# Performance work log

Measured on AMD Instinct MI355X. Metric: run time of the kernel, lower is better.

Reference implementation:

```python
import jax, jax.numpy as jnp
import numpy as np

SEQ_LEN, BATCH, VOCAB, EMB, HID, NUM_LAYERS = 128, 64, 10000, 512, 512, 2


def setup_inputs() -> dict:
    key = jax.random.key(0)
    ks = jax.random.split(key, 16)
    b = float(np.sqrt(1.0 / HID))  # Linear init bound per init_weights_uniform
    u = lambda k, shape, bound: jax.random.uniform(k, shape, jnp.float32, -bound, bound)
    L = NUM_LAYERS - 1
    return {
        "inputs": jax.random.randint(ks[0], (SEQ_LEN, BATCH), 0, VOCAB, dtype=jnp.int32),
        "hidden": jnp.zeros((NUM_LAYERS, BATCH, HID), jnp.float32),
        "emb": u(ks[1], (VOCAB, EMB), 0.1),
        "W_ih0": u(ks[2], (HID, EMB), b),
        "b_ih0": u(ks[3], (HID,), b),
        "W_hh0": u(ks[4], (HID, HID), b),
        "b_hh0": u(ks[5], (HID,), b),
        "W_in": u(ks[6], (L, HID, HID), b),
        "b_in": u(ks[7], (L, HID), b),
        "W_hh": u(ks[8], (L, HID, HID), b),
        "b_hh": u(ks[9], (L, HID), b),
        "Wy": u(ks[10], (VOCAB, HID), 0.1),
        "by": jnp.zeros((VOCAB,), jnp.float32),
    }


def reference(inputs, hidden, emb, W_ih0, b_ih0, W_hh0, b_hh0,
              W_in, b_in, W_hh, b_hh, Wy, by):
    n_extra = W_in.shape[0]  # num_layers - 1 (static)

    def step(h, x_t):
        # h: [L, B, H]; x_t: [B] int tokens
        e = emb[x_t]  # [B, E]
        h0 = jnp.tanh(e @ W_ih0.T + b_ih0 + h[0] @ W_hh0.T + b_hh0)
        hs = [h0]
        for l in range(n_extra):  # small static layer loop
            hl = jnp.tanh(hs[-1] @ W_in[l].T + b_in[l]
                          + h[l + 1] @ W_hh[l].T + b_hh[l])
            hs.append(hl)
        h_new = jnp.stack(hs)  # [L, B, H]
        logits_t = hs[-1] @ Wy.T + by  # [B, V]
        return h_new, logits_t

    hidden_final, logits = jax.lax.scan(step, hidden, inputs)
    return logits, hidden_final  # [S, B, V], [L, B, H]
```

## Files before the change

### kernel.cpp

```cpp
#include <hip/hip_runtime.h>
#include <hip/hip_bf16.h>

#define SEQ 128
#define BAT 64
#define VOC 10000
#define EMBD 512
#define HID 512
#define BH (BAT*HID)
#define PRE0_OFF 0
#define H0_OFF   ((size_t)SEQ*BH)
#define H1_OFF   (H0_OFF + (size_t)(SEQ+1)*BH)
#define FLAGS_OFF (H1_OFF + (size_t)(SEQ+1)*BH)
#define CONV_OFF (FLAGS_OFF + 256)
#define LOGITS_N ((size_t)SEQ*BAT*VOC)
#define CONV_USHORTS 5382144ull
#define WS_NEED_FLOATS (CONV_OFF + CONV_USHORTS/2)

typedef __attribute__((ext_vector_type(8))) __bf16 bf16x8;
typedef __attribute__((ext_vector_type(4))) float f32x4;

__global__ __launch_bounds__(256) void init_state_k(const float* __restrict__ hidden,
                                                    float* __restrict__ h0_0,
                                                    float* __restrict__ h1_0,
                                                    unsigned* __restrict__ flags) {
    int i = blockIdx.x * 256 + threadIdx.x;
    if (i < 256) flags[i] = 0u;
    if (i < BH) { h0_0[i] = hidden[i]; h1_0[i] = hidden[BH + i]; }
}

__global__ __launch_bounds__(256) void gemm_nt_k(
    const float* __restrict__ A, const int* __restrict__ tok,
    const float* __restrict__ Bm,
    const float* __restrict__ bias0, const float* __restrict__ bias1,
    float* __restrict__ C, int N, int K, int ldc)
{
    __shared__ float As[32][132];
    __shared__ float Bs[32][132];
    __shared__ int toks[128];

    const int tid = threadIdx.x;
    const int r0 = blockIdx.x * 128;
    const int c0 = blockIdx.y * 128;

    if (tok != nullptr && tid < 128) toks[tid] = tok[r0 + tid];
    __syncthreads();

    const int tn = tid & 15;
    const int tm = tid >> 4;
    const int m0 = tm * 8, n0 = tn * 8;

    float acc[8][8];
#pragma unroll
    for (int i = 0; i < 8; ++i)
#pragma unroll
        for (int j = 0; j < 8; ++j) acc[i][j] = 0.f;

    for (int k0 = 0; k0 < K; k0 += 32) {
#pragma unroll
        for (int p = 0; p < 4; ++p) {
            int idx = p * 256 + tid;
            int row = idx >> 3;
            int kq  = (idx & 7) << 2;
            size_t arow = tok ? (size_t)toks[row] : (size_t)(r0 + row);
            float4 a = *(const float4*)(A + arow * (size_t)K + k0 + kq);
            As[kq+0][row] = a.x; As[kq+1][row] = a.y;
            As[kq+2][row] = a.z; As[kq+3][row] = a.w;
            int gc = c0 + row;
            float4 b = make_float4(0.f, 0.f, 0.f, 0.f);
            if (gc < N) b = *(const float4*)(Bm + (size_t)gc * K + k0 + kq);
            Bs[kq+0][row] = b.x; Bs[kq+1][row] = b.y;
            Bs[kq+2][row] = b.z; Bs[kq+3][row] = b.w;
        }
        __syncthreads();
#pragma unroll 8
        for (int k = 0; k < 32; ++k) {
            float4 a0 = *(const float4*)&As[k][m0];
            float4 a1 = *(const float4*)&As[k][m0 + 4];
            float4 b0 = *(const float4*)&Bs[k][n0];
            float4 b1 = *(const float4*)&Bs[k][n0 + 4];
            float am[8] = {a0.x,a0.y,a0.z,a0.w,a1.x,a1.y,a1.z,a1.w};
            float bn[8] = {b0.x,b0.y,b0.z,b0.w,b1.x,b1.y,b1.z,b1.w};
#pragma unroll
            for (int i = 0; i < 8; ++i)
#pragma unroll
                for (int j = 0; j < 8; ++j) acc[i][j] += am[i] * bn[j];
        }
        __syncthreads();
    }

    const bool full = (c0 + 128 <= N);
#pragma unroll
    for (int i = 0; i < 8; ++i) {
        size_t r = (size_t)(r0 + m0 + i);
        float* crow = C + r * (size_t)ldc;
#pragma unroll
        for (int j = 0; j < 8; ++j) {
            int c = c0 + n0 + j;
            if (full || c < N) {
                float v = acc[i][j];
                if (bias0) v += bias0[c];
                if (bias1) v += bias1[c];
                crow[c] = v;
            }
        }
    }
}

#define BFLY(S, N)                                                     \
    {                                                                  \
        _Pragma("unroll")                                              \
        for (int i = 0; i < N; ++i) {                                  \
            float lo_ = a[i], hi_ = a[i + N];                          \
            float send_ = (lane & S) ? lo_ : hi_;                      \
            float recv_ = __shfl_xor(send_, S);                       \
            a[i] = ((lane & S) ? hi_ : lo_) + recv_;                   \
        }                                                              \
    }

__global__ __launch_bounds__(512) void recurrence_k(
    const float* __restrict__ pre0, const float* __restrict__ W_hh0,
    const float* __restrict__ W_in, const float* __restrict__ b_in,
    const float* __restrict__ W_hh, const float* __restrict__ b_hh,
    float* __restrict__ h0_all, float* __restrict__ h1_all,
    unsigned* __restrict__ flags)
{
    __shared__ float xs[16384];

    const int tid  = threadIdx.x;
    const int lane = tid & 63;
    const int wv   = tid >> 6;
    const int p = ((lane&1)<<5)|((lane&2)<<3)|((lane&4)<<1)
                | ((lane&8)>>1)|((lane&16)>>3)|((lane&32)>>5);
    const int b_own = p >> 3, j_own = p & 7;

    unsigned* fl1 = flags;
    unsigned* fl2 = flags + 64;

    float4 wr[8][2];
    float a[64];

    if (blockIdx.x < 64) {
        const int g = blockIdx.x >> 4, jb = blockIdx.x & 15;
        const int bt = wv & 1, jt = wv >> 1;
        const size_t win = (size_t)(g << 4) * HID;
#pragma unroll
        for (int jj = 0; jj < 8; ++jj) {
            const float* wp = W_hh0 + (size_t)(jb*32 + jt*8 + jj) * HID;
            wr[jj][0] = *(const float4*)(wp + lane*4);
            wr[jj][1] = *(const float4*)(wp + 256 + lane*4);
        }
        const unsigned* grp = fl1 + (g << 4);
        unsigned* myf = fl1 + (g << 4) + jb;
        const int bg = (g << 4) + (bt << 3) + b_own;
        const int jg = jb*32 + jt*8 + j_own;

        for (unsigned t = 1; t <= SEQ; ++t) {
            float pf = pre0[(size_t)(t-1)*BH + (size_t)bg*HID + jg];
            for (;;) {
                unsigned v = __hip_atomic_load(&grp[lane & 15], __ATOMIC_RELAXED,
                                               __HIP_MEMORY_SCOPE_AGENT);
                if (__ballot(v < (t - 1)) == 0ull) break;
            }
            __syncthreads();
            {
                const float4* src = (const float4*)(h0_all + (size_t)(t-1)*BH + win);
                float4 r0_, r1_, r2_, r3_;
                asm volatile("global_load_dwordx4 %0, %1, off sc0 sc1" : "=v"(r0_) : "v"(src + tid));
                asm volatile("global_load_dwordx4 %0, %1, off sc0 sc1" : "=v"(r1_) : "v"(src + tid + 512));
                asm volatile("global_load_dwordx4 %0, %1, off sc0 sc1" : "=v"(r2_) : "v"(src + tid + 1024));
                asm volatile("global_load_dwordx4 %0, %1, off sc0 sc1" : "=v"(r3_) : "v"(src + tid + 1536));
                asm volatile("s_waitcnt vmcnt(0)" ::: "memory");
                __builtin_amdgcn_sched_barrier(0);
                float4* dst = (float4*)xs;
                dst[tid] = r0_; dst[tid+512] = r1_; dst[tid+1024] = r2_; dst[tid+1536] = r3_;
            }
            __syncthreads();
#pragma unroll
            for (int i = 0; i < 64; ++i) a[i] = 0.f;
#pragma unroll
            for (int b = 0; b < 8; ++b) {
                const int row = (bt << 3) + b;
                float4 ha = *(const float4*)&xs[row*512 + lane*4];
                float4 hb = *(const float4*)&xs[row*512 + 256 + lane*4];
#pragma unroll
                for (int jj = 0; jj < 8; ++jj) {
                    a[b*8+jj] += ha.x*wr[jj][0].x + ha.y*wr[jj][0].y
                               + ha.z*wr[jj][0].z + ha.w*wr[jj][0].w
                               + hb.x*wr[jj][1].x + hb.y*wr[jj][1].y
                               + hb.z*wr[jj][1].z + hb.w*wr[jj][1].w;
                }
            }
            BFLY(1,32) BFLY(2,16) BFLY(4,8) BFLY(8,4) BFLY(16,2) BFLY(32,1)
            float v = tanhf(a[0] + pf);
            __hip_atomic_store(&h0_all[(size_t)t*BH + (size_t)bg*HID + jg], v,
                               __ATOMIC_RELAXED, __HIP_MEMORY_SCOPE_AGENT);
            asm volatile("s_waitcnt vmcnt(0)" ::: "memory");
            __syncthreads();
            if (tid == 0) __hip_atomic_store(myf, t, __ATOMIC_RELAXED,
                                             __HIP_MEMORY_SCOPE_AGENT);
        }
    } else {
        const int idx = blockIdx.x - 64;
        const int g = idx >> 5, jb = idx & 31;
        const int bt = wv & 1, jt = (wv >> 1) & 1, kt = wv >> 2;
        const size_t win = (size_t)(g << 4) * HID;
        const float* Wmat = kt ? W_hh : W_in;
#pragma unroll
        for (int jj = 0; jj < 8; ++jj) {
            const float* wp = Wmat + (size_t)(jb*16 + jt*8 + jj) * HID;
            wr[jj][0] = *(const float4*)(wp + lane*4);
            wr[jj][1] = *(const float4*)(wp + 256 + lane*4);
        }
        const unsigned* grpA = fl1 + (g << 4);
        const unsigned* grpB = fl2 + (g << 5);
        unsigned* myf = fl2 + (g << 5) + jb;
        const int bg = (g << 4) + (bt << 3) + b_own;
        const int jg = jb*16 + jt*8 + j_own;
        const float bias = b_in[jg] + b_hh[jg];
        const int scx = (wv & 3) * 64 + lane;

        for (unsigned t = 1; t <= SEQ; ++t) {
            for (;;) {
                unsigned v1 = __hip_atomic_load(&grpA[lane & 15], __ATOMIC_RELAXED,
                                                __HIP_MEMORY_SCOPE_AGENT);
                unsigned v2 = __hip_atomic_load(&grpB[lane & 31], __ATOMIC_RELAXED,
                                                __HIP_MEMORY_SCOPE_AGENT);
                if (__ballot(v1 < t) == 0ull && __ballot(v2 < (t - 1)) == 0ull) break;
            }
            __syncthreads();
            {
                const int q = tid & 255;
                const float4* src = (tid < 256)
                    ? (const float4*)(h0_all + (size_t)t*BH + win)
                    : (const float4*)(h1_all + (size_t)(t-1)*BH + win);
                float4 rr[8];
#pragma unroll
                for (int i = 0; i < 8; ++i)
                    asm volatile("global_load_dwordx4 %0, %1, off sc0 sc1"
                                 : "=v"(rr[i]) : "v"(src + q + i*256));
                asm volatile("s_waitcnt vmcnt(0)" ::: "memory");
                __builtin_amdgcn_sched_barrier(0);
                float4* dst = (float4*)(xs + ((tid < 256) ? 0 : 8192));
#pragma unroll
                for (int i = 0; i < 8; ++i) dst[q + i*256] = rr[i];
            }
            __syncthreads();
#pragma unroll
            for (int i = 0; i < 64; ++i) a[i] = 0.f;
            const float* xsrc = xs + (kt ? 8192 : 0);
#pragma unroll
            for (int b = 0; b < 8; ++b) {
                const int row = (bt << 3) + b;
                float4 ha = *(const float4*)&xsrc[row*512 + lane*4];
                float4 hb = *(const float4*)&xsrc[row*512 + 256 + lane*4];
#pragma unroll
                for (int jj = 0; jj < 8; ++jj) {
                    a[b*8+jj] += ha.x*wr[jj][0].x + ha.y*wr[jj][0].y
                               + ha.z*wr[jj][0].z + ha.w*wr[jj][0].w
                               + hb.x*wr[jj][1].x + hb.y*wr[jj][1].y
                               + hb.z*wr[jj][1].z + hb.w*wr[jj][1].w;
                }
            }
            BFLY(1,32) BFLY(2,16) BFLY(4,8) BFLY(8,4) BFLY(16,2) BFLY(32,1)
            __syncthreads();
            if (kt) xs[scx] = a[0];
            __syncthreads();
            if (!kt) {
                float v = tanhf(a[0] + xs[scx] + bias);
                __hip_atomic_store(&h1_all[(size_t)t*BH + (size_t)bg*HID + jg], v,
                                   __ATOMIC_RELAXED, __HIP_MEMORY_SCOPE_AGENT);
            }
            asm volatile("s_waitcnt vmcnt(0)" ::: "memory");
            __syncthreads();
            if (tid == 0) __hip_atomic_store(myf, t, __ATOMIC_RELAXED,
                                             __HIP_MEMORY_SCOPE_AGENT);
        }
    }
}

__global__ __launch_bounds__(256) void copy_out_k(const float* __restrict__ h0_all,
                                                  const float* __restrict__ h1_all,
                                                  float* __restrict__ out_hidden) {
    int g = blockIdx.x * 256 + threadIdx.x;
    if (g < BH)            out_hidden[g] = h0_all[(size_t)SEQ * BH + g];
    else if (g < 2 * BH)   out_hidden[g] = h1_all[(size_t)SEQ * BH + (g - BH)];
}


__device__ __forceinline__ unsigned bf16_rne(float x) {
    unsigned u = __float_as_uint(x);
    unsigned r = u + 0x7fffu + ((u >> 16) & 1u);
    return r >> 16;
}

__global__ __launch_bounds__(256) void split_hi_k(const float* __restrict__ src,
                                                  unsigned short* __restrict__ hi,
                                                  int n4) {
    int i = blockIdx.x * 256 + threadIdx.x;
    if (i >= n4) return;
    float4 v = ((const float4*)src)[i];
    ushort4 h4;
    h4.x = (unsigned short)bf16_rne(v.x); h4.y = (unsigned short)bf16_rne(v.y);
    h4.z = (unsigned short)bf16_rne(v.z); h4.w = (unsigned short)bf16_rne(v.w);
    ((ushort4*)hi)[i] = h4;
}

__global__ __launch_bounds__(256) void gemm_mfma2f_k(
    const float* __restrict__ Ag, const int* __restrict__ tok,
    const unsigned short* __restrict__ Bhg,
    const float* __restrict__ bias0, const float* __restrict__ bias1,
    float* __restrict__ C, int N, int ldc)
{
    __shared__ __align__(16) unsigned short sAh[128*64];
    __shared__ __align__(16) unsigned short sAl[128*64];
    __shared__ __align__(16) unsigned short sBh[128*64];

    const int tid = threadIdx.x;
    const int flat = blockIdx.y * gridDim.x + blockIdx.x;
    const int cpx  = (gridDim.x * gridDim.y) >> 3;
    const int w    = (flat & 7) * cpx + (flat >> 3);
    const int r0 = (w & 63) * 128, c0 = (w >> 6) * 128;

    const int lane = tid & 63, wvv = tid >> 6;
    const int mh = wvv >> 1, nh = wvv & 1;

    f32x4 acc[4][4];
#pragma unroll
    for (int i = 0; i < 4; ++i)
#pragma unroll
        for (int j = 0; j < 4; ++j) acc[i][j] = (f32x4){0.f, 0.f, 0.f, 0.f};

    const int srow = tid >> 1, shalf = tid & 1;
    const size_t arow = tok ? (size_t)tok[r0 + srow] : (size_t)(r0 + srow);
    const size_t abase = arow * 512 + (size_t)shalf * 32;
    const int brow = c0 + srow;
    const bool bok = brow < N;
    const size_t bbase = (size_t)(bok ? brow : 0) * 512 + shalf * 32;
    const int woff = srow * 64;
    const int swz = srow & 7;

    float4 fa[4][2];
    uint4 vbh[4];
#pragma unroll
    for (int g = 0; g < 4; ++g) {
        fa[g][0] = *(const float4*)(Ag + abase + g*8);
        fa[g][1] = *(const float4*)(Ag + abase + g*8 + 4);
        vbh[g]   = bok ? *(const uint4*)(Bhg + bbase + g*8) : (uint4){0,0,0,0};
    }

    for (int k0 = 0; k0 < 512; k0 += 64) {
        __syncthreads();
#pragma unroll
        for (int g = 0; g < 4; ++g) {
            float f[8] = {fa[g][0].x, fa[g][0].y, fa[g][0].z, fa[g][0].w,
                          fa[g][1].x, fa[g][1].y, fa[g][1].z, fa[g][1].w};
            unsigned hh[8], ll[8];
#pragma unroll
            for (int q = 0; q < 8; ++q) {
                hh[q] = bf16_rne(f[q]);
                ll[q] = bf16_rne(f[q] - __uint_as_float(hh[q] << 16));
            }
            uint4 ph = { hh[0] | (hh[1]<<16), hh[2] | (hh[3]<<16),
                         hh[4] | (hh[5]<<16), hh[6] | (hh[7]<<16) };
            uint4 pl = { ll[0] | (ll[1]<<16), ll[2] | (ll[3]<<16),
                         ll[4] | (ll[5]<<16), ll[6] | (ll[7]<<16) };
            int off = woff + (((shalf*4 + g) ^ swz) * 8);
            *(uint4*)&sAh[off] = ph;
            *(uint4*)&sAl[off] = pl;
            *(uint4*)&sBh[off] = vbh[g];
        }
        __syncthreads();
        if (k0 < 448) {
            const int kn = k0 + 64;
#pragma unroll
            for (int g = 0; g < 4; ++g) {
                fa[g][0] = *(const float4*)(Ag + abase + kn + g*8);
                fa[g][1] = *(const float4*)(Ag + abase + kn + g*8 + 4);
                vbh[g]   = bok ? *(const uint4*)(Bhg + bbase + kn + g*8) : (uint4){0,0,0,0};
            }
        }
#pragma unroll
        for (int c = 0; c < 2; ++c) {
            const int ks = ((c*4 + (lane >> 4)) ^ (lane & 7)) * 8;
            bf16x8 fAh[4], fAl[4], fBh[4];
#pragma unroll
            for (int mi = 0; mi < 4; ++mi) {
                int ro = (mh*64 + mi*16 + (lane & 15)) * 64;
                fAh[mi] = *(const bf16x8*)&sAh[ro + ks];
                fAl[mi] = *(const bf16x8*)&sAl[ro + ks];
            }
#pragma unroll
            for (int ni = 0; ni < 4; ++ni) {
                int ro = (nh*64 + ni*16 + (lane & 15)) * 64;
                fBh[ni] = *(const bf16x8*)&sBh[ro + ks];
            }
#pragma unroll
            for (int mi = 0; mi < 4; ++mi)
#pragma unroll
                for (int ni = 0; ni < 4; ++ni) {
                    acc[mi][ni] = __builtin_amdgcn_mfma_f32_16x16x32_bf16(
                        fAh[mi], fBh[ni], acc[mi][ni], 0, 0, 0);
                    acc[mi][ni] = __builtin_amdgcn_mfma_f32_16x16x32_bf16(
                        fAl[mi], fBh[ni], acc[mi][ni], 0, 0, 0);
                }
        }
    }

#pragma unroll
    for (int ni = 0; ni < 4; ++ni) {
        int gcol = c0 + nh*64 + ni*16 + (lane & 15);
        bool ok = gcol < N;
        float bias = 0.f;
        if (ok) {
            if (bias0) bias += bias0[gcol];
            if (bias1) bias += bias1[gcol];
        }
#pragma unroll
        for (int mi = 0; mi < 4; ++mi) {
            int grow = r0 + mh*64 + mi*16 + ((lane >> 4) << 2);
#pragma unroll
            for (int r = 0; r < 4; ++r)
                if (ok) C[(size_t)(grow + r) * ldc + gcol] = acc[mi][ni][r] + bias;
        }
    }
}

__global__ __launch_bounds__(256) void gemm_mfma1f_k(
    const float* __restrict__ Ag,
    const unsigned short* __restrict__ Bhg,
    const float* __restrict__ bias0,
    float* __restrict__ C, int N, int ldc)
{
    __shared__ __align__(16) unsigned short sAh[128*64];
    __shared__ __align__(16) unsigned short sBh[128*64];

    const int tid = threadIdx.x;
    const int flat = blockIdx.y * gridDim.x + blockIdx.x;
    const int cpx  = (gridDim.x * gridDim.y) >> 3;
    const int w    = (flat & 7) * cpx + (flat >> 3);
    const int r0 = (w & 63) * 128, c0 = (w >> 6) * 128;

    const int lane = tid & 63, wvv = tid >> 6;
    const int mh = wvv >> 1, nh = wvv & 1;

    f32x4 acc[4][4];
#pragma unroll
    for (int i = 0; i < 4; ++i)
#pragma unroll
        for (int j = 0; j < 4; ++j) acc[i][j] = (f32x4){0.f, 0.f, 0.f, 0.f};

    const int srow = tid >> 1, shalf = tid & 1;
    const size_t abase = (size_t)(r0 + srow) * 512 + (size_t)shalf * 32;
    const int brow = c0 + srow;
    const bool bok = brow < N;
    const size_t bbase = (size_t)(bok ? brow : 0) * 512 + shalf * 32;
    const int woff = srow * 64;
    const int swz = srow & 7;

    float4 fa[4][2];
    uint4 vbh[4];
#pragma unroll
    for (int g = 0; g < 4; ++g) {
        fa[g][0] = *(const float4*)(Ag + abase + g*8);
        fa[g][1] = *(const float4*)(Ag + abase + g*8 + 4);
        vbh[g]   = bok ? *(const uint4*)(Bhg + bbase + g*8) : (uint4){0,0,0,0};
    }

    for (int k0 = 0; k0 < 512; k0 += 64) {
        __syncthreads();
#pragma unroll
        for (int g = 0; g < 4; ++g) {
            float f[8] = {fa[g][0].x, fa[g][0].y, fa[g][0].z, fa[g][0].w,
                          fa[g][1].x, fa[g][1].y, fa[g][1].z, fa[g][1].w};
            unsigned hh[8];
#pragma unroll
            for (int q = 0; q < 8; ++q) hh[q] = bf16_rne(f[q]);
            uint4 ph = { hh[0] | (hh[1]<<16), hh[2] | (hh[3]<<16),
                         hh[4] | (hh[5]<<16), hh[6] | (hh[7]<<16) };
            int off = woff + (((shalf*4 + g) ^ swz) * 8);
            *(uint4*)&sAh[off] = ph;
            *(uint4*)&sBh[off] = vbh[g];
        }
        __syncthreads();
        if (k0 < 448) {
            const int kn = k0 + 64;
#pragma unroll
            for (int g = 0; g < 4; ++g) {
                fa[g][0] = *(const float4*)(Ag + abase + kn + g*8);
                fa[g][1] = *(const float4*)(Ag + abase + kn + g*8 + 4);
                vbh[g]   = bok ? *(const uint4*)(Bhg + bbase + kn + g*8) : (uint4){0,0,0,0};
            }
        }
#pragma unroll
        for (int c = 0; c < 2; ++c) {
            const int ks = ((c*4 + (lane >> 4)) ^ (lane & 7)) * 8;
            bf16x8 fAh[4], fBh[4];
#pragma unroll
            for (int mi = 0; mi < 4; ++mi) {
                int ro = (mh*64 + mi*16 + (lane & 15)) * 64;
                fAh[mi] = *(const bf16x8*)&sAh[ro + ks];
            }
#pragma unroll
            for (int ni = 0; ni < 4; ++ni) {
                int ro = (nh*64 + ni*16 + (lane & 15)) * 64;
                fBh[ni] = *(const bf16x8*)&sBh[ro + ks];
            }
#pragma unroll
            for (int mi = 0; mi < 4; ++mi)
#pragma unroll
                for (int ni = 0; ni < 4; ++ni)
                    acc[mi][ni] = __builtin_amdgcn_mfma_f32_16x16x32_bf16(
                        fAh[mi], fBh[ni], acc[mi][ni], 0, 0, 0);
        }
    }

#pragma unroll
    for (int ni = 0; ni < 4; ++ni) {
        int gcol = c0 + nh*64 + ni*16 + (lane & 15);
        bool ok = gcol < N;
        float bias = ok ? bias0[gcol] : 0.f;
#pragma unroll
        for (int mi = 0; mi < 4; ++mi) {
            int grow = r0 + mh*64 + mi*16 + ((lane >> 4) << 2);
#pragma unroll
            for (int r = 0; r < 4; ++r)
                if (ok) C[(size_t)(grow + r) * ldc + gcol] = acc[mi][ni][r] + bias;
        }
    }
}

extern "C" void kernel_launch(void* const* d_in, const int* in_sizes, int n_in,
                              void* d_out, int out_size, void* d_ws, size_t ws_size,
                              hipStream_t stream) {
    const int*   inputs = (const int*)d_in[0];
    const float* hidden = (const float*)d_in[1];
    const float* emb    = (const float*)d_in[2];
    const float* W_ih0  = (const float*)d_in[3];
    const float* b_ih0  = (const float*)d_in[4];
    const float* W_hh0  = (const float*)d_in[5];
    const float* b_hh0  = (const float*)d_in[6];
    const float* W_in   = (const float*)d_in[7];
    const float* b_in   = (const float*)d_in[8];
    const float* W_hh   = (const float*)d_in[9];
    const float* b_hh   = (const float*)d_in[10];
    const float* Wy     = (const float*)d_in[11];
    const float* by     = (const float*)d_in[12];
    float* out = (float*)d_out;

    float* ws     = (float*)d_ws;
    float* pre0   = ws + PRE0_OFF;
    float* h0_all = ws + H0_OFF;
    float* h1_all = ws + H1_OFF;
    unsigned* flags = (unsigned*)(ws + FLAGS_OFF);
    float* out_hidden = out + LOGITS_N;
    const bool big_ws = (ws_size >= WS_NEED_FLOATS * 4ull);

    unsigned short* wy_hi   = (unsigned short*)(ws + CONV_OFF);
    unsigned short* wih0_hi = wy_hi + (size_t)VOC * HID;

    init_state_k<<<dim3((BH + 255) / 256), dim3(256), 0, stream>>>(hidden, h0_all, h1_all, flags);

    if (big_ws) {
        split_hi_k<<<dim3(1024), dim3(256), 0, stream>>>(W_ih0, wih0_hi, HID*EMBD/4);
        split_hi_k<<<dim3(5000), dim3(256), 0, stream>>>(Wy, wy_hi, VOC*HID/4);
        gemm_mfma2f_k<<<dim3(64, 4), dim3(256), 0, stream>>>(
            emb, inputs, wih0_hi, b_ih0, b_hh0, pre0, HID, HID);
    } else {
        gemm_nt_k<<<dim3(64, 4), dim3(256), 0, stream>>>(
            emb, inputs, W_ih0, b_ih0, b_hh0, pre0, HID, EMBD, HID);
    }

    const float* pre0_c = pre0;
    void* kargs[] = { (void*)&pre0_c, (void*)&W_hh0, (void*)&W_in, (void*)&b_in,
                      (void*)&W_hh, (void*)&b_hh, (void*)&h0_all, (void*)&h1_all,
                      (void*)&flags };
    hipLaunchCooperativeKernel((const void*)recurrence_k, dim3(192), dim3(512),
                               kargs, 0, stream);

    copy_out_k<<<dim3(256), dim3(256), 0, stream>>>(h0_all, h1_all, out_hidden);

    if (big_ws) {
        gemm_mfma1f_k<<<dim3(64, 79), dim3(256), 0, stream>>>(
            h1_all + BH, wy_hi, by, out, VOC, VOC);
    } else {
        gemm_nt_k<<<dim3(64, 79), dim3(256), 0, stream>>>(
            h1_all + BH, nullptr, Wy, nullptr, by, out, VOC, HID, VOC);
    }
}
```

Baseline: 1.220 ms.

## Fuse output projection into recurrence kernel to overlap logits with timesteps

```diff
diff --git a/kernel.cpp b/kernel.cpp
--- a/kernel.cpp
+++ b/kernel.cpp
@@ -117,15 +117,19 @@
         }                                                              \
     }
 
-__global__ __launch_bounds__(512) void recurrence_k(
+__device__ __forceinline__ unsigned bf16_rne(float x) {
+    unsigned u = __float_as_uint(x);
+    unsigned r = u + 0x7fffu + ((u >> 16) & 1u);
+    return r >> 16;
+}
+
+__device__ __forceinline__ void recurrence_body(
     const float* __restrict__ pre0, const float* __restrict__ W_hh0,
     const float* __restrict__ W_in, const float* __restrict__ b_in,
     const float* __restrict__ W_hh, const float* __restrict__ b_hh,
     float* __restrict__ h0_all, float* __restrict__ h1_all,
-    unsigned* __restrict__ flags)
+    unsigned* __restrict__ flags, float* __restrict__ xs)
 {
-    __shared__ float xs[16384];
-
     const int tid  = threadIdx.x;
     const int lane = tid & 63;
     const int wv   = tid >> 6;
@@ -278,6 +282,120 @@
     }
 }
 
+__global__ __launch_bounds__(512) void recurrence_k(
+    const float* __restrict__ pre0, const float* __restrict__ W_hh0,
+    const float* __restrict__ W_in, const float* __restrict__ b_in,
+    const float* __restrict__ W_hh, const float* __restrict__ b_hh,
+    float* __restrict__ h0_all, float* __restrict__ h1_all,
+    unsigned* __restrict__ flags)
+{
+    __shared__ float xs[16384];
+    recurrence_body(pre0, W_hh0, W_in, b_in, W_hh, b_hh, h0_all, h1_all, flags, xs);
+}
+
+__global__ __launch_bounds__(512, 4) void rec_logits_k(
+    const float* __restrict__ pre0, const float* __restrict__ W_hh0,
+    const float* __restrict__ W_in, const float* __restrict__ b_in,
+    const float* __restrict__ W_hh, const float* __restrict__ b_hh,
+    float* __restrict__ h0_all, float* __restrict__ h1_all,
+    unsigned* __restrict__ flags,
+    const unsigned short* __restrict__ wy_hi, const float* __restrict__ by,
+    float* __restrict__ Cout)
+{
+    __shared__ float xs[16384];
+
+    if (blockIdx.x < 192) {
+        recurrence_body(pre0, W_hh0, W_in, b_in, W_hh, b_hh, h0_all, h1_all, flags, xs);
+        return;
+    }
+
+    const int tid  = threadIdx.x;
+    const int lane = tid & 63;
+    const int idx = blockIdx.x - 192;
+    int t, ts, tc;
+    if (idx < 96)       { t = idx + 1;                 ts = 0;        tc = 79; }
+    else if (idx < 144) { int q = idx - 96;  t = 97 + (q >> 1);  ts = (q & 1) * 40; tc = (q & 1) ? 39 : 40; }
+    else                { int q = idx - 144; t = 121 + (q >> 3); int h = q & 7; ts = h * 10; tc = (h == 7) ? 9 : 10; }
+
+    const unsigned* fl2p = flags + 64;
+    if (tid < 64) {
+        for (;;) {
+            unsigned v1 = __hip_atomic_load(&fl2p[lane], __ATOMIC_RELAXED,
+                                            __HIP_MEMORY_SCOPE_AGENT);
+            unsigned v2 = __hip_atomic_load(&fl2p[lane + 64], __ATOMIC_RELAXED,
+                                            __HIP_MEMORY_SCOPE_AGENT);
+            if (__ballot(v1 < (unsigned)t) == 0ull &&
+                __ballot(v2 < (unsigned)t) == 0ull) break;
+            __builtin_amdgcn_s_sleep(8);
+        }
+    }
+    __syncthreads();
+
+    unsigned short* sA = (unsigned short*)xs;
+    {
+        const float4* src = (const float4*)(h1_all + (size_t)t * BH);
+#pragma unroll
+        for (int r = 0; r < 2; ++r) {
+            float4 f[8];
+#pragma unroll
+            for (int i = 0; i < 4; ++i) {
+                const float4* p0 = src + 2 * (tid + (r * 4 + i) * 512);
+                asm volatile("global_load_dwordx4 %0, %1, off sc0 sc1" : "=v"(f[2*i])   : "v"(p0));
+                asm volatile("global_load_dwordx4 %0, %1, off sc0 sc1" : "=v"(f[2*i+1]) : "v"(p0 + 1));
+            }
+            asm volatile("s_waitcnt vmcnt(0)" ::: "memory");
+            __builtin_amdgcn_sched_barrier(0);
+#pragma unroll
+            for (int i = 0; i < 4; ++i) {
+                int c = tid + (r * 4 + i) * 512;
+                int row = c >> 6, kc = c & 63;
+                float v[8] = {f[2*i].x, f[2*i].y, f[2*i].z, f[2*i].w,
+                              f[2*i+1].x, f[2*i+1].y, f[2*i+1].z, f[2*i+1].w};
+                unsigned hh[8];
+#pragma unroll
+                for (int q2 = 0; q2 < 8; ++q2) hh[q2] = bf16_rne(v[q2]);
+                uint4 ph = {hh[0]|(hh[1]<<16), hh[2]|(hh[3]<<16),
+                            hh[4]|(hh[5]<<16), hh[6]|(hh[7]<<16)};
+                int byte = (kc * 16) ^ ((row & 7) << 4);
+                *(uint4*)((char*)sA + row * 1024 + byte) = ph;
+            }
+        }
+    }
+    __syncthreads();
+
+    const int w8 = tid >> 6;
+    const int l15 = lane & 15, l4 = lane >> 4;
+    for (int ct = ts; ct < ts + tc; ++ct) {
+        const int gcol = ct * 128 + w8 * 16 + l15;
+        const bool ok = gcol < VOC;
+        const unsigned short* bp = wy_hi + (size_t)(ok ? gcol : 0) * 512 + l4 * 8;
+        f32x4 acc[4];
+#pragma unroll
+        for (int mi = 0; mi < 4; ++mi) acc[mi] = (f32x4){0.f, 0.f, 0.f, 0.f};
+#pragma unroll
+        for (int kk = 0; kk < 16; ++kk) {
+            bf16x8 fB = *(const bf16x8*)(bp + kk * 32);
+#pragma unroll
+            for (int mi = 0; mi < 4; ++mi) {
+                int row = mi * 16 + l15;
+                int byte = (kk * 64 + l4 * 16) ^ ((row & 7) << 4);
+                bf16x8 fA = *(const bf16x8*)((char*)sA + row * 1024 + byte);
+                acc[mi] = __builtin_amdgcn_mfma_f32_16x16x32_bf16(fA, fB, acc[mi], 0, 0, 0);
+            }
+        }
+        if (ok) {
+            float bias = by[gcol];
+#pragma unroll
+            for (int mi = 0; mi < 4; ++mi) {
+                int grow = (t - 1) * 64 + mi * 16 + l4 * 4;
+#pragma unroll
+                for (int r2 = 0; r2 < 4; ++r2)
+                    Cout[(size_t)(grow + r2) * VOC + gcol] = acc[mi][r2] + bias;
+            }
+        }
+    }
+}
+
 __global__ __launch_bounds__(256) void copy_out_k(const float* __restrict__ h0_all,
                                                   const float* __restrict__ h1_all,
                                                   float* __restrict__ out_hidden) {
@@ -286,12 +404,6 @@
     else if (g < 2 * BH)   out_hidden[g] = h1_all[(size_t)SEQ * BH + (g - BH)];
 }
 
-
-__device__ __forceinline__ unsigned bf16_rne(float x) {
-    unsigned u = __float_as_uint(x);
-    unsigned r = u + 0x7fffu + ((u >> 16) & 1u);
-    return r >> 16;
-}
 
 __global__ __launch_bounds__(256) void split_hi_k(const float* __restrict__ src,
                                                   unsigned short* __restrict__ hi,
@@ -560,30 +672,46 @@
 
     init_state_k<<<dim3((BH + 255) / 256), dim3(256), 0, stream>>>(hidden, h0_all, h1_all, flags);
 
+    const float* pre0_c = pre0;
     if (big_ws) {
         split_hi_k<<<dim3(1024), dim3(256), 0, stream>>>(W_ih0, wih0_hi, HID*EMBD/4);
         split_hi_k<<<dim3(5000), dim3(256), 0, stream>>>(Wy, wy_hi, VOC*HID/4);
         gemm_mfma2f_k<<<dim3(64, 4), dim3(256), 0, stream>>>(
             emb, inputs, wih0_hi, b_ih0, b_hh0, pre0, HID, HID);
+
+        void* kargsF[] = { (void*)&pre0_c, (void*)&W_hh0, (void*)&W_in, (void*)&b_in,
+                           (void*)&W_hh, (void*)&b_hh, (void*)&h0_all, (void*)&h1_all,
+                           (void*)&flags, (void*)&wy_hi, (void*)&by, (void*)&out };
+        int nb = 0;
+        hipError_t oe = hipOccupancyMaxActiveBlocksPerMultiprocessor(
+            &nb, (const void*)rec_logits_k, 512, 0);
+        bool done = false;
+        if (oe == hipSuccess && (size_t)nb * 256 >= 400) {
+            hipError_t e = hipLaunchCooperativeKernel((const void*)rec_logits_k,
+                                                      dim3(400), dim3(512), kargsF, 0, stream);
+            if (e == hipSuccess) done = true;
+            else (void)hipGetLastError();
+        }
+        if (!done) {
+            void* kargs[] = { (void*)&pre0_c, (void*)&W_hh0, (void*)&W_in, (void*)&b_in,
+                              (void*)&W_hh, (void*)&b_hh, (void*)&h0_all, (void*)&h1_all,
+                              (void*)&flags };
+            hipLaunchCooperativeKernel((const void*)recurrence_k, dim3(192), dim3(512),
+                                       kargs, 0, stream);
+            gemm_mfma1f_k<<<dim3(64, 79), dim3(256), 0, stream>>>(
+                h1_all + BH, wy_hi, by, out, VOC, VOC);
+        }
     } else {
         gemm_nt_k<<<dim3(64, 4), dim3(256), 0, stream>>>(
             emb, inputs, W_ih0, b_ih0, b_hh0, pre0, HID, EMBD, HID);
-    }
-
-    const float* pre0_c = pre0;
-    void* kargs[] = { (void*)&pre0_c, (void*)&W_hh0, (void*)&W_in, (void*)&b_in,
-                      (void*)&W_hh, (void*)&b_hh, (void*)&h0_all, (void*)&h1_all,
-                      (void*)&flags };
-    hipLaunchCooperativeKernel((const void*)recurrence_k, dim3(192), dim3(512),
-                               kargs, 0, stream);
-
-    copy_out_k<<<dim3(256), dim3(256), 0, stream>>>(h0_all, h1_all, out_hidden);
-
-    if (big_ws) {
-        gemm_mfma1f_k<<<dim3(64, 79), dim3(256), 0, stream>>>(
-            h1_all + BH, wy_hi, by, out, VOC, VOC);
-    } else {
+        void* kargs[] = { (void*)&pre0_c, (void*)&W_hh0, (void*)&W_in, (void*)&b_in,
+                          (void*)&W_hh, (void*)&b_hh, (void*)&h0_all, (void*)&h1_all,
+                          (void*)&flags };
+        hipLaunchCooperativeKernel((const void*)recurrence_k, dim3(192), dim3(512),
+                                   kargs, 0, stream);
         gemm_nt_k<<<dim3(64, 79), dim3(256), 0, stream>>>(
             h1_all + BH, nullptr, Wy, nullptr, by, out, VOC, HID, VOC);
     }
-}
+
+    copy_out_k<<<dim3(256), dim3(256), 0, stream>>>(h0_all, h1_all, out_hidden);
+}
```

Result: no change. 1.221 ms (+0.1%).

## Place recurrence tasks on XCC-local blocks and drop sc1 on state loads

Applied to the files above, without the earlier changes.

```diff
diff --git a/kernel.cpp b/kernel.cpp
--- a/kernel.cpp
+++ b/kernel.cpp
@@ -117,6 +117,172 @@
         }                                                              \
     }
 
+__device__ __forceinline__ unsigned bf16_rne(float x) {
+    unsigned u = __float_as_uint(x);
+    unsigned r = u + 0x7fffu + ((u >> 16) & 1u);
+    return r >> 16;
+}
+
+__device__ __forceinline__ void recurrence_body(
+    int blk,
+    const float* __restrict__ pre0, const float* __restrict__ W_hh0,
+    const float* __restrict__ W_in, const float* __restrict__ b_in,
+    const float* __restrict__ W_hh, const float* __restrict__ b_hh,
+    float* __restrict__ h0_all, float* __restrict__ h1_all,
+    unsigned* __restrict__ flags, float* __restrict__ xs)
+{
+    const int tid  = threadIdx.x;
+    const int lane = tid & 63;
+    const int wv   = tid >> 6;
+    const int p = ((lane&1)<<5)|((lane&2)<<3)|((lane&4)<<1)
+                | ((lane&8)>>1)|((lane&16)>>3)|((lane&32)>>5);
+    const int b_own = p >> 3, j_own = p & 7;
+
+    unsigned* fl1 = flags;
+    unsigned* fl2 = flags + 64;
+
+    float4 wr[8][2];
+    float a[64];
+
+    if (blk < 64) {
+        const int g = blk >> 4, jb = blk & 15;
+        const int bt = wv & 1, jt = wv >> 1;
+        const size_t win = (size_t)(g << 4) * HID;
+#pragma unroll
+        for (int jj = 0; jj < 8; ++jj) {
+            const float* wp = W_hh0 + (size_t)(jb*32 + jt*8 + jj) * HID;
+            wr[jj][0] = *(const float4*)(wp + lane*4);
+            wr[jj][1] = *(const float4*)(wp + 256 + lane*4);
+        }
+        const unsigned* grp = fl1 + (g << 4);
+        unsigned* myf = fl1 + (g << 4) + jb;
+        const int bg = (g << 4) + (bt << 3) + b_own;
+        const int jg = jb*32 + jt*8 + j_own;
+
+        for (unsigned t = 1; t <= SEQ; ++t) {
+            float pf = pre0[(size_t)(t-1)*BH + (size_t)bg*HID + jg];
+            for (;;) {
+                unsigned v = __hip_atomic_load(&grp[lane & 15], __ATOMIC_RELAXED,
+                                               __HIP_MEMORY_SCOPE_AGENT);
+                if (__ballot(v < (t - 1)) == 0ull) break;
+            }
+            __syncthreads();
+            {
+                const float4* src = (const float4*)(h0_all + (size_t)(t-1)*BH + win);
+                float4 r0_, r1_, r2_, r3_;
+                asm volatile("global_load_dwordx4 %0, %1, off sc0" : "=v"(r0_) : "v"(src + tid));
+                asm volatile("global_load_dwordx4 %0, %1, off sc0" : "=v"(r1_) : "v"(src + tid + 512));
+                asm volatile("global_load_dwordx4 %0, %1, off sc0" : "=v"(r2_) : "v"(src + tid + 1024));
+                asm volatile("global_load_dwordx4 %0, %1, off sc0" : "=v"(r3_) : "v"(src + tid + 1536));
+                asm volatile("s_waitcnt vmcnt(0)" ::: "memory");
+                __builtin_amdgcn_sched_barrier(0);
+                float4* dst = (float4*)xs;
+                dst[tid] = r0_; dst[tid+512] = r1_; dst[tid+1024] = r2_; dst[tid+1536] = r3_;
+            }
+            __syncthreads();
+#pragma unroll
+            for (int i = 0; i < 64; ++i) a[i] = 0.f;
+#pragma unroll
+            for (int b = 0; b < 8; ++b) {
+                const int row = (bt << 3) + b;
+                float4 ha = *(const float4*)&xs[row*512 + lane*4];
+                float4 hb = *(const float4*)&xs[row*512 + 256 + lane*4];
+#pragma unroll
+                for (int jj = 0; jj < 8; ++jj) {
+                    a[b*8+jj] += ha.x*wr[jj][0].x + ha.y*wr[jj][0].y
+                               + ha.z*wr[jj][0].z + ha.w*wr[jj][0].w
+                               + hb.x*wr[jj][1].x + hb.y*wr[jj][1].y
+                               + hb.z*wr[jj][1].z + hb.w*wr[jj][1].w;
+                }
+            }
+            BFLY(1,32) BFLY(2,16) BFLY(4,8) BFLY(8,4) BFLY(16,2) BFLY(32,1)
+            float v = tanhf(a[0] + pf);
+            __hip_atomic_store(&h0_all[(size_t)t*BH + (size_t)bg*HID + jg], v,
+                               __ATOMIC_RELAXED, __HIP_MEMORY_SCOPE_AGENT);
+            asm volatile("s_waitcnt vmcnt(0)" ::: "memory");
+            __syncthreads();
+            if (tid == 0) __hip_atomic_store(myf, t, __ATOMIC_RELAXED,
+                                             __HIP_MEMORY_SCOPE_AGENT);
+        }
+    } else {
+        const int idx = blk - 64;
+        const int g = idx >> 5, jb = idx & 31;
+        const int bt = wv & 1, jt = (wv >> 1) & 1, kt = wv >> 2;
+        const size_t win = (size_t)(g << 4) * HID;
+        const float* Wmat = kt ? W_hh : W_in;
+#pragma unroll
+        for (int jj = 0; jj < 8; ++jj) {
+            const float* wp = Wmat + (size_t)(jb*16 + jt*8 + jj) * HID;
+            wr[jj][0] = *(const float4*)(wp + lane*4);
+            wr[jj][1] = *(const float4*)(wp + 256 + lane*4);
+        }
+        const unsigned* grpA = fl1 + (g << 4);
+        const unsigned* grpB = fl2 + (g << 5);
+        unsigned* myf = fl2 + (g << 5) + jb;
+        const int bg = (g << 4) + (bt << 3) + b_own;
+        const int jg = jb*16 + jt*8 + j_own;
+        const float bias = b_in[jg] + b_hh[jg];
+        const int scx = (wv & 3) * 64 + lane;
+
+        for (unsigned t = 1; t <= SEQ; ++t) {
+            for (;;) {
+                unsigned v1 = __hip_atomic_load(&grpA[lane & 15], __ATOMIC_RELAXED,
+                                                __HIP_MEMORY_SCOPE_AGENT);
+                unsigned v2 = __hip_atomic_load(&grpB[lane & 31], __ATOMIC_RELAXED,
+                                                __HIP_MEMORY_SCOPE_AGENT);
+                if (__ballot(v1 < t) == 0ull && __ballot(v2 < (t - 1)) == 0ull) break;
+            }
+            __syncthreads();
+            {
+                const int q = tid & 255;
+                const float4* src = (tid < 256)
+                    ? (const float4*)(h0_all + (size_t)t*BH + win)
+                    : (const float4*)(h1_all + (size_t)(t-1)*BH + win);
+                float4 rr[8];
+#pragma unroll
+                for (int i = 0; i < 8; ++i)
+                    asm volatile("global_load_dwordx4 %0, %1, off sc0"
+                                 : "=v"(rr[i]) : "v"(src + q + i*256));
+                asm volatile("s_waitcnt vmcnt(0)" ::: "memory");
+                __builtin_amdgcn_sched_barrier(0);
+                float4* dst = (float4*)(xs + ((tid < 256) ? 0 : 8192));
+#pragma unroll
+                for (int i = 0; i < 8; ++i) dst[q + i*256] = rr[i];
+            }
+            __syncthreads();
+#pragma unroll
+            for (int i = 0; i < 64; ++i) a[i] = 0.f;
+            const float* xsrc = xs + (kt ? 8192 : 0);
+#pragma unroll
+            for (int b = 0; b < 8; ++b) {
+                const int row = (bt << 3) + b;
+                float4 ha = *(const float4*)&xsrc[row*512 + lane*4];
+                float4 hb = *(const float4*)&xsrc[row*512 + 256 + lane*4];
+#pragma unroll
+                for (int jj = 0; jj < 8; ++jj) {
+                    a[b*8+jj] += ha.x*wr[jj][0].x + ha.y*wr[jj][0].y
+                               + ha.z*wr[jj][0].z + ha.w*wr[jj][0].w
+                               + hb.x*wr[jj][1].x + hb.y*wr[jj][1].y
+                               + hb.z*wr[jj][1].z + hb.w*wr[jj][1].w;
+                }
+            }
+            BFLY(1,32) BFLY(2,16) BFLY(4,8) BFLY(8,4) BFLY(16,2) BFLY(32,1)
+            __syncthreads();
+            if (kt) xs[scx] = a[0];
+            __syncthreads();
+            if (!kt) {
+                float v = tanhf(a[0] + xs[scx] + bias);
+                __hip_atomic_store(&h1_all[(size_t)t*BH + (size_t)bg*HID + jg], v,
+                                   __ATOMIC_RELAXED, __HIP_MEMORY_SCOPE_AGENT);
+            }
+            asm volatile("s_waitcnt vmcnt(0)" ::: "memory");
+            __syncthreads();
+            if (tid == 0) __hip_atomic_store(myf, t, __ATOMIC_RELAXED,
+                                             __HIP_MEMORY_SCOPE_AGENT);
+        }
+    }
+}
+
 __global__ __launch_bounds__(512) void recurrence_k(
     const float* __restrict__ pre0, const float* __restrict__ W_hh0,
     const float* __restrict__ W_in, const float* __restrict__ b_in,
@@ -125,157 +291,46 @@
     unsigned* __restrict__ flags)
 {
     __shared__ float xs[16384];
-
-    const int tid  = threadIdx.x;
-    const int lane = tid & 63;
-    const int wv   = tid >> 6;
-    const int p = ((lane&1)<<5)|((lane&2)<<3)|((lane&4)<<1)
-                | ((lane&8)>>1)|((lane&16)>>3)|((lane&32)>>5);
-    const int b_own = p >> 3, j_own = p & 7;
-
-    unsigned* fl1 = flags;
-    unsigned* fl2 = flags + 64;
-
-    float4 wr[8][2];
-    float a[64];
-
-    if (blockIdx.x < 64) {
-        const int g = blockIdx.x >> 4, jb = blockIdx.x & 15;
-        const int bt = wv & 1, jt = wv >> 1;
-        const size_t win = (size_t)(g << 4) * HID;
-#pragma unroll
-        for (int jj = 0; jj < 8; ++jj) {
-            const float* wp = W_hh0 + (size_t)(jb*32 + jt*8 + jj) * HID;
-            wr[jj][0] = *(const float4*)(wp + lane*4);
-            wr[jj][1] = *(const float4*)(wp + 256 + lane*4);
-        }
-        const unsigned* grp = fl1 + (g << 4);
-        unsigned* myf = fl1 + (g << 4) + jb;
-        const int bg = (g << 4) + (bt << 3) + b_own;
-        const int jg = jb*32 + jt*8 + j_own;
-
-        for (unsigned t = 1; t <= SEQ; ++t) {
-            float pf = pre0[(size_t)(t-1)*BH + (size_t)bg*HID + jg];
-            for (;;) {
-                unsigned v = __hip_atomic_load(&grp[lane & 15], __ATOMIC_RELAXED,
-                                               __HIP_MEMORY_SCOPE_AGENT);
-                if (__ballot(v < (t - 1)) == 0ull) break;
-            }
-            __syncthreads();
-            {
-                const float4* src = (const float4*)(h0_all + (size_t)(t-1)*BH + win);
-                float4 r0_, r1_, r2_, r3_;
-                asm volatile("global_load_dwordx4 %0, %1, off sc0 sc1" : "=v"(r0_) : "v"(src + tid));
-                asm volatile("global_load_dwordx4 %0, %1, off sc0 sc1" : "=v"(r1_) : "v"(src + tid + 512));
-                asm volatile("global_load_dwordx4 %0, %1, off sc0 sc1" : "=v"(r2_) : "v"(src + tid + 1024));
-                asm volatile("global_load_dwordx4 %0, %1, off sc0 sc1" : "=v"(r3_) : "v"(src + tid + 1536));
-                asm volatile("s_waitcnt vmcnt(0)" ::: "memory");
-                __builtin_amdgcn_sched_barrier(0);
-                float4* dst = (float4*)xs;
-                dst[tid] = r0_; dst[tid+512] = r1_; dst[tid+1024] = r2_; dst[tid+1536] = r3_;
-            }
-            __syncthreads();
-#pragma unroll
-            for (int i = 0; i < 64; ++i) a[i] = 0.f;
-#pragma unroll
-            for (int b = 0; b < 8; ++b) {
-                const int row = (bt << 3) + b;
-                float4 ha = *(const float4*)&xs[row*512 + lane*4];
-                float4 hb = *(const float4*)&xs[row*512 + 256 + lane*4];
-#pragma unroll
-                for (int jj = 0; jj < 8; ++jj) {
-                    a[b*8+jj] += ha.x*wr[jj][0].x + ha.y*wr[jj][0].y
-                               + ha.z*wr[jj][0].z + ha.w*wr[jj][0].w
-                               + hb.x*wr[jj][1].x + hb.y*wr[jj][1].y
-                               + hb.z*wr[jj][1].z + hb.w*wr[jj][1].w;
-                }
-            }
-            BFLY(1,32) BFLY(2,16) BFLY(4,8) BFLY(8,4) BFLY(16,2) BFLY(32,1)
-            float v = tanhf(a[0] + pf);
-            __hip_atomic_store(&h0_all[(size_t)t*BH + (size_t)bg*HID + jg], v,
-                               __ATOMIC_RELAXED, __HIP_MEMORY_SCOPE_AGENT);
-            asm volatile("s_waitcnt vmcnt(0)" ::: "memory");
-            __syncthreads();
-            if (tid == 0) __hip_atomic_store(myf, t, __ATOMIC_RELAXED,
-                                             __HIP_MEMORY_SCOPE_AGENT);
-        }
-    } else {
-        const int idx = blockIdx.x - 64;
-        const int g = idx >> 5, jb = idx & 31;
-        const int bt = wv & 1, jt = (wv >> 1) & 1, kt = wv >> 2;
-        const size_t win = (size_t)(g << 4) * HID;
-        const float* Wmat = kt ? W_hh : W_in;
-#pragma unroll
-        for (int jj = 0; jj < 8; ++jj) {
-            const float* wp = Wmat + (size_t)(jb*16 + jt*8 + jj) * HID;
-            wr[jj][0] = *(const float4*)(wp + lane*4);
-            wr[jj][1] = *(const float4*)(wp + 256 + lane*4);
-        }
-        const unsigned* grpA = fl1 + (g << 4);
-        const unsigned* grpB = fl2 + (g << 5);
-        unsigned* myf = fl2 + (g << 5) + jb;
-        const int bg = (g << 4) + (bt << 3) + b_own;
-        const int jg = jb*16 + jt*8 + j_own;
-        const float bias = b_in[jg] + b_hh[jg];
-        const int scx = (wv & 3) * 64 + lane;
-
-        for (unsigned t = 1; t <= SEQ; ++t) {
-            for (;;) {
-                unsigned v1 = __hip_atomic_load(&grpA[lane & 15], __ATOMIC_RELAXED,
-                                                __HIP_MEMORY_SCOPE_AGENT);
-                unsigned v2 = __hip_atomic_load(&grpB[lane & 31], __ATOMIC_RELAXED,
-                                                __HIP_MEMORY_SCOPE_AGENT);
-                if (__ballot(v1 < t) == 0ull && __ballot(v2 < (t - 1)) == 0ull) break;
-            }
-            __syncthreads();
-            {
-                const int q = tid & 255;
-                const float4* src = (tid < 256)
-                    ? (const float4*)(h0_all + (size_t)t*BH + win)
-                    : (const float4*)(h1_all + (size_t)(t-1)*BH + win);
-                float4 rr[8];
-#pragma unroll
-                for (int i = 0; i < 8; ++i)
-                    asm volatile("global_load_dwordx4 %0, %1, off sc0 sc1"
-                                 : "=v"(rr[i]) : "v"(src + q + i*256));
-                asm volatile("s_waitcnt vmcnt(0)" ::: "memory");
-                __builtin_amdgcn_sched_barrier(0);
-                float4* dst = (float4*)(xs + ((tid < 256) ? 0 : 8192));
-#pragma unroll
-                for (int i = 0; i < 8; ++i) dst[q + i*256] = rr[i];
-            }
-            __syncthreads();
-#pragma unroll
-            for (int i = 0; i < 64; ++i) a[i] = 0.f;
-            const float* xsrc = xs + (kt ? 8192 : 0);
-#pragma unroll
-            for (int b = 0; b < 8; ++b) {
-                const int row = (bt << 3) + b;
-                float4 ha = *(const float4*)&xsrc[row*512 + lane*4];
-                float4 hb = *(const float4*)&xsrc[row*512 + 256 + lane*4];
-#pragma unroll
-                for (int jj = 0; jj < 8; ++jj) {
-                    a[b*8+jj] += ha.x*wr[jj][0].x + ha.y*wr[jj][0].y
-                               + ha.z*wr[jj][0].z + ha.w*wr[jj][0].w
-                               + hb.x*wr[jj][1].x + hb.y*wr[jj][1].y
-                               + hb.z*wr[jj][1].z + hb.w*wr[jj][1].w;
-                }
-            }
-            BFLY(1,32) BFLY(2,16) BFLY(4,8) BFLY(8,4) BFLY(16,2) BFLY(32,1)
-            __syncthreads();
-            if (kt) xs[scx] = a[0];
-            __syncthreads();
-            if (!kt) {
-                float v = tanhf(a[0] + xs[scx] + bias);
-                __hip_atomic_store(&h1_all[(size_t)t*BH + (size_t)bg*HID + jg], v,
-                                   __ATOMIC_RELAXED, __HIP_MEMORY_SCOPE_AGENT);
-            }
-            asm volatile("s_waitcnt vmcnt(0)" ::: "memory");
-            __syncthreads();
-            if (tid == 0) __hip_atomic_store(myf, t, __ATOMIC_RELAXED,
-                                             __HIP_MEMORY_SCOPE_AGENT);
-        }
-    }
+    recurrence_body(blockIdx.x, pre0, W_hh0, W_in, b_in, W_hh, b_hh,
+                    h0_all, h1_all, flags, xs);
+}
+
+__global__ __launch_bounds__(512) void recurrence9_k(
+    const float* __restrict__ pre0, const float* __restrict__ W_hh0,
+    const float* __restrict__ W_in, const float* __restrict__ b_in,
+    const float* __restrict__ W_hh, const float* __restrict__ b_hh,
+    float* __restrict__ h0_all, float* __restrict__ h1_all,
+    unsigned* __restrict__ flags)
+{
+    __shared__ float xs[16384];
+    __shared__ int s_task;
+
+    if (threadIdx.x == 0) {
+        unsigned xcc;
+        asm volatile("s_getreg_b32 %0, hwreg(20, 0, 4)" : "=s"(xcc));
+        unsigned* q = flags + 192;
+        int task = -1;
+        if (xcc < 4u) {
+            unsigned r = atomicAdd(&q[xcc], 1u);
+            if (r < 48u) task = (r < 16u) ? (int)(xcc*16u + r)
+                                          : (int)(64u + xcc*32u + (r - 16u));
+        }
+        if (task < 0) {
+            __builtin_amdgcn_s_sleep(127);
+            for (unsigned g = 0; g < 4u && task < 0; ++g) {
+                unsigned r = atomicAdd(&q[g], 1u);
+                if (r < 48u) task = (r < 16u) ? (int)(g*16u + r)
+                                              : (int)(64u + g*32u + (r - 16u));
+            }
+        }
+        s_task = task;
+    }
+    __syncthreads();
+    const int task = s_task;
+    if (task < 0) return;
+
+    recurrence_body(task, pre0, W_hh0, W_in, b_in, W_hh, b_hh,
+                    h0_all, h1_all, flags, xs);
 }
 
 __global__ __launch_bounds__(256) void copy_out_k(const float* __restrict__ h0_all,
@@ -287,22 +342,22 @@
 }
 
 
-__device__ __forceinline__ unsigned bf16_rne(float x) {
-    unsigned u = __float_as_uint(x);
-    unsigned r = u + 0x7fffu + ((u >> 16) & 1u);
-    return r >> 16;
-}
-
-__global__ __launch_bounds__(256) void split_hi_k(const float* __restrict__ src,
-                                                  unsigned short* __restrict__ hi,
-                                                  int n4) {
+__global__ __launch_bounds__(256) void split2_hi_k(const float* __restrict__ wy,
+                                                   const float* __restrict__ wih0,
+                                                   unsigned short* __restrict__ wy_hi,
+                                                   unsigned short* __restrict__ wih0_hi) {
+    const int n4a = VOC*HID/4;
+    const int n4b = HID*EMBD/4;
     int i = blockIdx.x * 256 + threadIdx.x;
-    if (i >= n4) return;
-    float4 v = ((const float4*)src)[i];
+    const float* src; unsigned short* dst; int idx;
+    if (i < n4a)            { src = wy;   dst = wy_hi;   idx = i; }
+    else if (i < n4a + n4b) { src = wih0; dst = wih0_hi; idx = i - n4a; }
+    else return;
+    float4 v = ((const float4*)src)[idx];
     ushort4 h4;
     h4.x = (unsigned short)bf16_rne(v.x); h4.y = (unsigned short)bf16_rne(v.y);
     h4.z = (unsigned short)bf16_rne(v.z); h4.w = (unsigned short)bf16_rne(v.w);
-    ((ushort4*)hi)[i] = h4;
+    ((ushort4*)dst)[idx] = h4;
 }
 
 __global__ __launch_bounds__(256) void gemm_mfma2f_k(
@@ -560,29 +615,36 @@
 
     init_state_k<<<dim3((BH + 255) / 256), dim3(256), 0, stream>>>(hidden, h0_all, h1_all, flags);
 
+    const float* pre0_c = pre0;
     if (big_ws) {
-        split_hi_k<<<dim3(1024), dim3(256), 0, stream>>>(W_ih0, wih0_hi, HID*EMBD/4);
-        split_hi_k<<<dim3(5000), dim3(256), 0, stream>>>(Wy, wy_hi, VOC*HID/4);
+        split2_hi_k<<<dim3((VOC*HID/4 + HID*EMBD/4 + 255) / 256), dim3(256), 0, stream>>>(
+            Wy, W_ih0, wy_hi, wih0_hi);
         gemm_mfma2f_k<<<dim3(64, 4), dim3(256), 0, stream>>>(
             emb, inputs, wih0_hi, b_ih0, b_hh0, pre0, HID, HID);
+
+        void* kargs9[] = { (void*)&pre0_c, (void*)&W_hh0, (void*)&W_in, (void*)&b_in,
+                           (void*)&W_hh, (void*)&b_hh, (void*)&h0_all, (void*)&h1_all,
+                           (void*)&flags };
+        hipError_t e = hipLaunchCooperativeKernel((const void*)recurrence9_k,
+                                                  dim3(384), dim3(512), kargs9, 0, stream);
+        if (e != hipSuccess) {
+            (void)hipGetLastError();
+            hipLaunchCooperativeKernel((const void*)recurrence_k, dim3(192), dim3(512),
+                                       kargs9, 0, stream);
+        }
+
+        copy_out_k<<<dim3(256), dim3(256), 0, stream>>>(h0_all, h1_all, out_hidden);
+        gemm_mfma1f_k<<<dim3(64, 79), dim3(256), 0, stream>>>(
+            h1_all + BH, wy_hi, by, out, VOC, VOC);
     } else {
         gemm_nt_k<<<dim3(64, 4), dim3(256), 0, stream>>>(
             emb, inputs, W_ih0, b_ih0, b_hh0, pre0, HID, EMBD, HID);
-    }
-
-    const float* pre0_c = pre0;
-    void* kargs[] = { (void*)&pre0_c, (void*)&W_hh0, (void*)&W_in, (void*)&b_in,
-                      (void*)&W_hh, (void*)&b_hh, (void*)&h0_all, (void*)&h1_all,
-                      (void*)&flags };
-    hipLaunchCooperativeKernel((const void*)recurrence_k, dim3(192), dim3(512),
-                               kargs, 0, stream);
-
-    copy_out_k<<<dim3(256), dim3(256), 0, stream>>>(h0_all, h1_all, out_hidden);
-
-    if (big_ws) {
-        gemm_mfma1f_k<<<dim3(64, 79), dim3(256), 0, stream>>>(
-            h1_all + BH, wy_hi, by, out, VOC, VOC);
-    } else {
+        void* kargs[] = { (void*)&pre0_c, (void*)&W_hh0, (void*)&W_in, (void*)&b_in,
+                          (void*)&W_hh, (void*)&b_hh, (void*)&h0_all, (void*)&h1_all,
+                          (void*)&flags };
+        hipLaunchCooperativeKernel((const void*)recurrence_k, dim3(192), dim3(512),
+                                   kargs, 0, stream);
+        copy_out_k<<<dim3(256), dim3(256), 0, stream>>>(h0_all, h1_all, out_hidden);
         gemm_nt_k<<<dim3(64, 79), dim3(256), 0, stream>>>(
             h1_all + BH, nullptr, Wy, nullptr, by, out, VOC, HID, VOC);
     }
```

After: 1.122 ms. 8.0% less time.
